# Kernel optimization log

Hardware: AMD Instinct MI355X
Metric: run time of the kernel (lower is better)

Reference implementation:

```python
import jax, jax.numpy as jnp
import numpy as np

T = 300  # windowsize = windowstep(50) * windowmul(6)
D_IN = 39
H1, H2 = 35, 30
FC1, FC2, OUT = 50, 40, 2


def _lstm_layer(x_tbd, W, b, H):
    """TF LSTMCell: gates ordered i, j, f, o; forget_bias=1.0; tanh activation.
    x_tbd: [T, B, D]; W: [D+H, 4H]; b: [4H]. Returns hidden states [T, B, H]."""
    B = x_tbd.shape[1]
    h0 = jnp.zeros((B, H), x_tbd.dtype)
    c0 = jnp.zeros((B, H), x_tbd.dtype)

    def step(carry, xt):
        h, c = carry
        z = jnp.concatenate([xt, h], axis=-1) @ W + b  # [B, 4H]
        i, j, f, o = jnp.split(z, 4, axis=-1)
        c = jax.nn.sigmoid(f + 1.0) * c + jax.nn.sigmoid(i) * jnp.tanh(j)
        h = jax.nn.sigmoid(o) * jnp.tanh(c)
        return (h, c), h

    _, hs = jax.lax.scan(step, (h0, c0), x_tbd)
    return hs


def _stack(x_tbd, W1, b1, W2, b2):
    h1 = _lstm_layer(x_tbd, W1, b1, H1)
    return _lstm_layer(h1, W2, b2, H2)


def setup_inputs() -> dict:
    key = jax.random.key(0)
    ks = jax.random.split(key, 16)
    B = 4096
    s = lambda fan_in: 1.0 / np.sqrt(fan_in)

    def mat(k, shape):
        return jax.random.normal(k, shape, jnp.float32) * s(shape[0])

    return {
        "x": jax.random.normal(ks[0], (B, T, D_IN), jnp.float32),
        "fw_W1": mat(ks[1], (D_IN + H1, 4 * H1)), "fw_b1": jnp.zeros((4 * H1,), jnp.float32),
        "fw_W2": mat(ks[2], (H1 + H2, 4 * H2)), "fw_b2": jnp.zeros((4 * H2,), jnp.float32),
        "bw_W1": mat(ks[3], (D_IN + H1, 4 * H1)), "bw_b1": jnp.zeros((4 * H1,), jnp.float32),
        "bw_W2": mat(ks[4], (H1 + H2, 4 * H2)), "bw_b2": jnp.zeros((4 * H2,), jnp.float32),
        "W_fc1": mat(ks[5], (2 * H2, FC1)), "b_fc1": jnp.zeros((FC1,), jnp.float32),
        "W_fc2": mat(ks[6], (FC1, FC2)), "b_fc2": jnp.zeros((FC2,), jnp.float32),
        "W_out": mat(ks[7], (FC2, OUT)), "b_out": jnp.zeros((OUT,), jnp.float32),
    }


def reference(x, fw_W1, fw_b1, fw_W2, fw_b2, bw_W1, bw_b1, bw_W2, bw_b2,
              W_fc1, b_fc1, W_fc2, b_fc2, W_out, b_out):
    x_tbd = jnp.transpose(x, (1, 0, 2))  # [T, B, D]
    h_fw = _stack(x_tbd, fw_W1, fw_b1, fw_W2, fw_b2)               # [T, B, H2]
    h_bw = _stack(x_tbd[::-1], bw_W1, bw_b1, bw_W2, bw_b2)[::-1]   # [T, B, H2]
    h = jnp.concatenate([h_fw, h_bw], axis=-1)  # [T, B, 2*H2]
    h = jnp.transpose(h, (1, 0, 2))             # [B, T, 60]
    h = jax.nn.relu(h @ W_fc1 + b_fc1)
    h = jax.nn.relu(h @ W_fc2 + b_fc2)
    logits = h @ W_out + b_out                  # [B, T, 2]
    return logits
```

## Files before the change

### kernel.cpp

```cpp
#include <hip/hip_runtime.h>


#define T_STEPS 300
#define DIN 39
#define H1 35
#define H2 30
#define BATCH 4096
#define FC1N 50
#define FC2N 40

#define PAN_STR 136

typedef _Float16 f16;
typedef _Float16 half8 __attribute__((ext_vector_type(8)));
typedef float floatx4 __attribute__((ext_vector_type(4)));

__device__ __forceinline__ float sigf(float x) {
    return __builtin_amdgcn_rcpf(1.0f + __expf(-x));
}
__device__ __forceinline__ float sig_tanh(float a, float b) {
    float bc = fminf(b, 30.0f);
    float ea = __expf(-a);
    float E  = __expf(2.0f * bc);
    return (E - 1.0f) * __builtin_amdgcn_rcpf((1.0f + ea) * (E + 1.0f));
}

__global__ void wprep_kernel(const float* __restrict__ fw1, const float* __restrict__ bw1,
                             const float* __restrict__ fw2, const float* __restrict__ bw2,
                             f16* __restrict__ bp) {
    int frag = blockIdx.x;
    int lane = threadIdx.x;
    int dir = frag / 60;
    int rem = frag % 60;
    int layer = (rem < 36) ? 0 : 1;
    int r2 = (layer == 0) ? rem : rem - 36;
    int ug = r2 / 12, g = (r2 % 12) / 3, c = r2 % 3;
    int u = ug * 16 + (lane & 15);
    const float* W = (layer == 0) ? (dir ? bw1 : fw1) : (dir ? bw2 : fw2);
    for (int j = 0; j < 8; ++j) {
        int k = c * 32 + (lane >> 4) * 8 + j;
        float v = 0.0f;
        if (layer == 0) {
            if (u < H1) {
                int kr = (k < 39) ? k : ((k >= 40 && k < 75) ? k - 1 : -1);
                if (kr >= 0) v = W[kr * (4 * H1) + g * H1 + u];
            }
        } else {
            if (u < H2 && k < 65) v = W[k * (4 * H2) + g * H2 + u];
        }
        bp[(size_t)frag * 512 + lane * 8 + j] = (f16)v;
    }
}

__global__ void fcwprep_kernel(const float* __restrict__ Wf1, const float* __restrict__ Wf2,
                               const float* __restrict__ Wo, f16* __restrict__ fcp) {
    int f = blockIdx.x;
    int lane = threadIdx.x;
    int lm = lane & 15, oct = lane >> 4;
    for (int j = 0; j < 8; ++j) {
        float v = 0.0f;
        if (f < 8) {
            int tile = f >> 1, chunk = f & 1;
            int n = tile * 16 + lm;
            int kl = oct * 8 + j;
            if (n < FC1N && kl < 30) v = Wf1[(chunk * 30 + kl) * FC1N + n];
        } else if (f < 14) {
            int g = f - 8, tile = g >> 1, chunk = g & 1;
            int n = tile * 16 + lm;
            int k = chunk * 32 + oct * 8 + j;
            if (n < FC2N && k < FC1N) v = Wf2[k * FC2N + n];
        } else {
            int chunk = f - 14;
            int k = chunk * 32 + oct * 8 + j;
            if (lm < 2 && k < FC2N) v = Wo[k * 2 + lm];
        }
        fcp[(size_t)f * 512 + lane * 8 + j] = (f16)v;
    }
}

__global__ __launch_bounds__(320, 3) void lstm_fused(
    const float* __restrict__ x, const f16* __restrict__ bp,
    const float* __restrict__ fb1, const float* __restrict__ bb1,
    const float* __restrict__ fb2, const float* __restrict__ bb2,
    f16* __restrict__ h2s)
{
    __shared__ f16 pan[2][16 * PAN_STR];

    const int tid = threadIdx.x;
    const int b0  = blockIdx.x * 16;
    const int dir = blockIdx.y;
    const int wv   = tid >> 6;
    const int lane = tid & 63;
    const int lm = lane & 15, oct = lane >> 4;
    const bool isL2 = (wv >= 3);
    const int ug = isL2 ? (wv - 3) : wv;
    const int u  = ug * 16 + lm;
    const int Hn = isL2 ? H2 : H1;
    const float* bias = isL2 ? (dir ? bb2 : fb2) : (dir ? bb1 : fb1);
    const int fragbase = dir * 60 + (isL2 ? 36 : 0) + ug * 12;

    half8 bf[4][3];
    #pragma unroll
    for (int g = 0; g < 4; ++g)
        #pragma unroll
        for (int c = 0; c < 3; ++c)
            bf[g][c] = *(const half8*)(bp + (size_t)(fragbase + g * 3 + c) * 512 + lane * 8);

    float zb[4];
    #pragma unroll
    for (int g = 0; g < 4; ++g)
        zb[g] = (u < Hn) ? bias[g * Hn + u] : 0.f;
    float cst[4] = {0.f, 0.f, 0.f, 0.f};

    f16* h2p = h2s + ((size_t)(dir * BATCH + b0 + oct * 4) * T_STEPS
                      + (dir ? (T_STEPS - 1) : 0)) * 32 + u;
    const int h2step = dir ? -32 : 32;

    for (int idx = tid; idx < 16 * PAN_STR; idx += 320) {
        pan[0][idx] = (f16)0.f; pan[1][idx] = (f16)0.f;
    }
    __syncthreads();

    const int sr = tid / 10, sq = tid % 10;
    float xv[4] = {0.f, 0.f, 0.f, 0.f};
    if (tid < 160) {
        int t0 = dir ? (T_STEPS - 1) : 0;
        const float* p0 = x + ((size_t)(b0 + sr) * T_STEPS + t0) * DIN;
        union { f16 h[4]; uint2 u; } pk;
        #pragma unroll
        for (int i = 0; i < 4; ++i) { int k = sq * 4 + i; pk.h[i] = (k < DIN) ? (f16)p0[k] : (f16)0.f; }
        *(uint2*)(&pan[0][sr * PAN_STR + sq * 4]) = pk.u;
        int t1 = dir ? (T_STEPS - 2) : 1;
        const float* p1 = x + ((size_t)(b0 + sr) * T_STEPS + t1) * DIN;
        #pragma unroll
        for (int i = 0; i < 4; ++i) { int k = sq * 4 + i; xv[i] = (k < DIN) ? p1[k] : 0.f; }
    }
    __syncthreads();

    const int arow = lm * PAN_STR + oct * 8 + (isL2 ? 40 : 0);

    if (!isL2) {
        floatx4 C[4];
        #pragma unroll
        for (int g = 0; g < 4; ++g) C[g] = (floatx4){zb[g], zb[g], zb[g], zb[g]};
        half8 a0 = *(const half8*)(&pan[0][arow]);
        half8 a1 = *(const half8*)(&pan[0][arow + 32]);
        half8 a2 = *(const half8*)(&pan[0][arow + 64]);
        #pragma unroll
        for (int g = 0; g < 4; ++g) {
            C[g] = __builtin_amdgcn_mfma_f32_16x16x32_f16(a0, bf[g][0], C[g], 0, 0, 0);
            C[g] = __builtin_amdgcn_mfma_f32_16x16x32_f16(a1, bf[g][1], C[g], 0, 0, 0);
            C[g] = __builtin_amdgcn_mfma_f32_16x16x32_f16(a2, bf[g][2], C[g], 0, 0, 0);
        }
        #pragma unroll
        for (int r = 0; r < 4; ++r) {
            float cc = sigf(C[2][r] + 1.0f) * cst[r] + sig_tanh(C[0][r], C[1][r]);
            cst[r] = cc;
            float hh = sig_tanh(C[3][r], cc);
            if (u < H1) {
                int row = oct * 4 + r;
                pan[1][row * PAN_STR + 40 + u] = (f16)hh;
            }
        }
    }
    const float* px = x + ((size_t)(b0 + sr) * T_STEPS
                           + (dir ? (T_STEPS - 4) : 3)) * DIN + sq * 4;
    const int xstep = dir ? -DIN : DIN;
    if (tid < 160) {
        union { f16 h[4]; uint2 u; } pk;
        #pragma unroll
        for (int i = 0; i < 4; ++i) pk.h[i] = (f16)xv[i];
        *(uint2*)(&pan[1][sr * PAN_STR + sq * 4]) = pk.u;
        int t2 = dir ? (T_STEPS - 3) : 2;
        const float* p2 = x + ((size_t)(b0 + sr) * T_STEPS + t2) * DIN;
        #pragma unroll
        for (int i = 0; i < 4; ++i) { int k = sq * 4 + i; xv[i] = (k < DIN) ? p2[k] : 0.f; }
    }
    __syncthreads();

    for (int s = 0; s < T_STEPS; ++s) {
        const int p = 1 - (s & 1);

        float xn[4] = {0.f, 0.f, 0.f, 0.f};
        if (tid < 160) {
            #pragma unroll
            for (int i = 0; i < 4; ++i) { int k = sq * 4 + i; xn[i] = (k < DIN) ? px[i] : 0.f; }
        }
        if (s < T_STEPS - 4) px += xstep;

        const f16* ap = &pan[p][0];
        floatx4 C[4];
        #pragma unroll
        for (int g = 0; g < 4; ++g) C[g] = (floatx4){zb[g], zb[g], zb[g], zb[g]};
        {
            half8 a0 = *(const half8*)(ap + arow);
            half8 a1 = *(const half8*)(ap + arow + 32);
            half8 a2 = *(const half8*)(ap + arow + 64);
            #pragma unroll
            for (int g = 0; g < 4; ++g) {
                C[g] = __builtin_amdgcn_mfma_f32_16x16x32_f16(a0, bf[g][0], C[g], 0, 0, 0);
                C[g] = __builtin_amdgcn_mfma_f32_16x16x32_f16(a1, bf[g][1], C[g], 0, 0, 0);
                C[g] = __builtin_amdgcn_mfma_f32_16x16x32_f16(a2, bf[g][2], C[g], 0, 0, 0);
            }
        }

        f16* w = &pan[1 - p][0];
        if (!isL2) {
            #pragma unroll
            for (int r = 0; r < 4; ++r) {
                float cc = sigf(C[2][r] + 1.0f) * cst[r] + sig_tanh(C[0][r], C[1][r]);
                cst[r] = cc;
                float hh = sig_tanh(C[3][r], cc);
                if (u < H1) {
                    int row = oct * 4 + r;
                    w[row * PAN_STR + 40 + u] = (f16)hh;
                }
            }
        } else {
            #pragma unroll
            for (int r = 0; r < 4; ++r) {
                float dd = sigf(C[2][r] + 1.0f) * cst[r] + sig_tanh(C[0][r], C[1][r]);
                cst[r] = dd;
                float gg = sig_tanh(C[3][r], dd);
                int row = oct * 4 + r;
                f16 gv = (f16)gg;
                w[row * PAN_STR + 75 + u] = gv;
                h2p[(size_t)r * T_STEPS * 32] = gv;
            }
        }
        h2p += h2step;

        if (tid < 160) {
            union { f16 h[4]; uint2 u; } pk;
            #pragma unroll
            for (int i = 0; i < 4; ++i) pk.h[i] = (f16)xv[i];
            *(uint2*)(&pan[1 - p][sr * PAN_STR + sq * 4]) = pk.u;
            #pragma unroll
            for (int i = 0; i < 4; ++i) xv[i] = xn[i];
        }
        __syncthreads();
    }
}

__global__ __launch_bounds__(256) void fc_kernel(
    const f16* __restrict__ h2s, const f16* __restrict__ fcp,
    const float* __restrict__ bf1, const float* __restrict__ bf2,
    const float* __restrict__ bo, float* __restrict__ out)
{
    __shared__ f16 apf[4][2][16 * 72];
    const int tid = threadIdx.x;
    const int wv = tid >> 6, lane = tid & 63;
    const int lm = lane & 15, oct = lane >> 4;
    f16* pa = &apf[wv][0][0];
    f16* pb = &apf[wv][1][0];

    {
        uint* z = (uint*)pa;
        for (int i = lane; i < 1152; i += 64) z[i] = 0u;
    }

    half8 wf[16];
    #pragma unroll
    for (int f = 0; f < 16; ++f)
        wf[f] = *(const half8*)(fcp + (size_t)f * 512 + lane * 8);

    const int ar = lm * 72 + oct * 8;
    const size_t base = (size_t)blockIdx.x * 256 + wv * 64;
    const size_t bwoff = (size_t)BATCH * T_STEPS * 32;

    union U8 { uint4 u; half8 h; };
    const f16* gp = h2s + (base + lm) * 32 + oct * 8;
    U8 va, vb;
    va.u = *(const uint4*)gp;
    vb.u = *(const uint4*)(gp + bwoff);

    for (int it = 0; it < 4; ++it) {
        half8 a0 = va.h, a1 = vb.h;
        if (it < 3) {
            const f16* gn = gp + (size_t)(it + 1) * 16 * 32;
            va.u = *(const uint4*)gn;
            vb.u = *(const uint4*)(gn + bwoff);
        }

        floatx4 C[4];
        #pragma unroll
        for (int t = 0; t < 4; ++t) {
            int col = t * 16 + lm;
            float b = (col < FC1N) ? bf1[col] : 0.f;
            C[t] = (floatx4){b, b, b, b};
            C[t] = __builtin_amdgcn_mfma_f32_16x16x32_f16(a0, wf[t * 2 + 0], C[t], 0, 0, 0);
            C[t] = __builtin_amdgcn_mfma_f32_16x16x32_f16(a1, wf[t * 2 + 1], C[t], 0, 0, 0);
        }
        #pragma unroll
        for (int t = 0; t < 4; ++t) {
            int col = t * 16 + lm;
            #pragma unroll
            for (int r = 0; r < 4; ++r)
                pa[(oct * 4 + r) * 72 + col] = (f16)fmaxf(C[t][r], 0.f);
        }

        half8 b0 = *(const half8*)(pa + ar);
        half8 b1 = *(const half8*)(pa + ar + 32);
        floatx4 D[3];
        #pragma unroll
        for (int t = 0; t < 3; ++t) {
            int col = t * 16 + lm;
            float b = (col < FC2N) ? bf2[col] : 0.f;
            D[t] = (floatx4){b, b, b, b};
            D[t] = __builtin_amdgcn_mfma_f32_16x16x32_f16(b0, wf[8 + t * 2 + 0], D[t], 0, 0, 0);
            D[t] = __builtin_amdgcn_mfma_f32_16x16x32_f16(b1, wf[8 + t * 2 + 1], D[t], 0, 0, 0);
        }
        #pragma unroll
        for (int t = 0; t < 3; ++t) {
            int col = t * 16 + lm;
            #pragma unroll
            for (int r = 0; r < 4; ++r)
                pb[(oct * 4 + r) * 72 + col] = (f16)fmaxf(D[t][r], 0.f);
        }

        half8 c0 = *(const half8*)(pb + ar);
        half8 c1 = *(const half8*)(pb + ar + 32);
        float b = (lm < 2) ? bo[lm] : 0.f;
        floatx4 E = (floatx4){b, b, b, b};
        E = __builtin_amdgcn_mfma_f32_16x16x32_f16(c0, wf[14], E, 0, 0, 0);
        E = __builtin_amdgcn_mfma_f32_16x16x32_f16(c1, wf[15], E, 0, 0, 0);
        if (lm < 2) {
            const size_t rid0 = base + it * 16;
            #pragma unroll
            for (int r = 0; r < 4; ++r)
                out[(rid0 + oct * 4 + r) * 2 + lm] = E[r];
        }
    }
}

extern "C" void kernel_launch(void* const* d_in, const int* in_sizes, int n_in,
                              void* d_out, int out_size, void* d_ws, size_t ws_size,
                              hipStream_t stream) {
    const float* x     = (const float*)d_in[0];
    const float* fw_W1 = (const float*)d_in[1];
    const float* fw_b1 = (const float*)d_in[2];
    const float* fw_W2 = (const float*)d_in[3];
    const float* fw_b2 = (const float*)d_in[4];
    const float* bw_W1 = (const float*)d_in[5];
    const float* bw_b1 = (const float*)d_in[6];
    const float* bw_W2 = (const float*)d_in[7];
    const float* bw_b2 = (const float*)d_in[8];
    const float* Wf1   = (const float*)d_in[9];
    const float* bf1   = (const float*)d_in[10];
    const float* Wf2   = (const float*)d_in[11];
    const float* bf2   = (const float*)d_in[12];
    const float* Wo    = (const float*)d_in[13];
    const float* bo    = (const float*)d_in[14];
    float* outp = (float*)d_out;

    f16* h2s = (f16*)d_ws;
    f16* bp  = h2s + (size_t)2 * BATCH * T_STEPS * 32;
    f16* fcp = bp + (size_t)120 * 512;

    wprep_kernel<<<120, 64, 0, stream>>>(fw_W1, bw_W1, fw_W2, bw_W2, bp);
    fcwprep_kernel<<<16, 64, 0, stream>>>(Wf1, Wf2, Wo, fcp);

    dim3 gl(BATCH / 16, 2);
    lstm_fused<<<gl, 320, 0, stream>>>(x, bp, fw_b1, bw_b1, fw_b2, bw_b2, h2s);

    fc_kernel<<<(BATCH * T_STEPS) / 256, 256, 0, stream>>>(
        h2s, fcp, bf1, bf2, bo, outp);
}
```

Measured before the change: 699.4 us.

## Process 32 batch rows per LSTM block with two interleaved MFMA tiles

Measured after the change: 803.8 us. 14.9% more time.

```diff
diff --git a/kernel.cpp b/kernel.cpp
--- a/kernel.cpp
+++ b/kernel.cpp
@@ -10,6 +10,7 @@
 #define FC2N 40
 
 #define PAN_STR 136
+#define ROWS 32
 
 typedef _Float16 f16;
 typedef _Float16 half8 __attribute__((ext_vector_type(8)));
@@ -78,16 +79,16 @@
     }
 }
 
-__global__ __launch_bounds__(320, 3) void lstm_fused(
+__global__ __launch_bounds__(320, 1) void lstm_fused(
     const float* __restrict__ x, const f16* __restrict__ bp,
     const float* __restrict__ fb1, const float* __restrict__ bb1,
     const float* __restrict__ fb2, const float* __restrict__ bb2,
     f16* __restrict__ h2s)
 {
-    __shared__ f16 pan[2][16 * PAN_STR];
+    __shared__ f16 pan[2][ROWS * PAN_STR];
 
     const int tid = threadIdx.x;
-    const int b0  = blockIdx.x * 16;
+    const int b0  = blockIdx.x * ROWS;
     const int dir = blockIdx.y;
     const int wv   = tid >> 6;
     const int lane = tid & 63;
@@ -110,20 +111,22 @@
     #pragma unroll
     for (int g = 0; g < 4; ++g)
         zb[g] = (u < Hn) ? bias[g * Hn + u] : 0.f;
-    float cst[4] = {0.f, 0.f, 0.f, 0.f};
+    float cs1[4] = {0.f, 0.f, 0.f, 0.f};
+    float cs2[4] = {0.f, 0.f, 0.f, 0.f};
 
     f16* h2p = h2s + ((size_t)(dir * BATCH + b0 + oct * 4) * T_STEPS
                       + (dir ? (T_STEPS - 1) : 0)) * 32 + u;
+    f16* h2q = h2p + (size_t)16 * T_STEPS * 32;
     const int h2step = dir ? -32 : 32;
 
-    for (int idx = tid; idx < 16 * PAN_STR; idx += 320) {
+    for (int idx = tid; idx < ROWS * PAN_STR; idx += 320) {
         pan[0][idx] = (f16)0.f; pan[1][idx] = (f16)0.f;
     }
     __syncthreads();
 
     const int sr = tid / 10, sq = tid % 10;
-    float xv[4] = {0.f, 0.f, 0.f, 0.f};
-    if (tid < 160) {
+    float xv[4];
+    {
         int t0 = dir ? (T_STEPS - 1) : 0;
         const float* p0 = x + ((size_t)(b0 + sr) * T_STEPS + t0) * DIN;
         union { f16 h[4]; uint2 u; } pk;
@@ -137,36 +140,50 @@
     }
     __syncthreads();
 
-    const int arow = lm * PAN_STR + oct * 8 + (isL2 ? 40 : 0);
+    const int arow1 = lm * PAN_STR + oct * 8 + (isL2 ? 40 : 0);
+    const int arow2 = arow1 + 16 * PAN_STR;
 
     if (!isL2) {
-        floatx4 C[4];
-        #pragma unroll
-        for (int g = 0; g < 4; ++g) C[g] = (floatx4){zb[g], zb[g], zb[g], zb[g]};
-        half8 a0 = *(const half8*)(&pan[0][arow]);
-        half8 a1 = *(const half8*)(&pan[0][arow + 32]);
-        half8 a2 = *(const half8*)(&pan[0][arow + 64]);
+        floatx4 C1[4], C2[4];
         #pragma unroll
         for (int g = 0; g < 4; ++g) {
-            C[g] = __builtin_amdgcn_mfma_f32_16x16x32_f16(a0, bf[g][0], C[g], 0, 0, 0);
-            C[g] = __builtin_amdgcn_mfma_f32_16x16x32_f16(a1, bf[g][1], C[g], 0, 0, 0);
-            C[g] = __builtin_amdgcn_mfma_f32_16x16x32_f16(a2, bf[g][2], C[g], 0, 0, 0);
+            C1[g] = (floatx4){zb[g], zb[g], zb[g], zb[g]};
+            C2[g] = C1[g];
+        }
+        half8 a10 = *(const half8*)(&pan[0][arow1]);
+        half8 a11 = *(const half8*)(&pan[0][arow1 + 32]);
+        half8 a12 = *(const half8*)(&pan[0][arow1 + 64]);
+        half8 a20 = *(const half8*)(&pan[0][arow2]);
+        half8 a21 = *(const half8*)(&pan[0][arow2 + 32]);
+        half8 a22 = *(const half8*)(&pan[0][arow2 + 64]);
+        #pragma unroll
+        for (int g = 0; g < 4; ++g) {
+            C1[g] = __builtin_amdgcn_mfma_f32_16x16x32_f16(a10, bf[g][0], C1[g], 0, 0, 0);
+            C1[g] = __builtin_amdgcn_mfma_f32_16x16x32_f16(a11, bf[g][1], C1[g], 0, 0, 0);
+            C1[g] = __builtin_amdgcn_mfma_f32_16x16x32_f16(a12, bf[g][2], C1[g], 0, 0, 0);
+            C2[g] = __builtin_amdgcn_mfma_f32_16x16x32_f16(a20, bf[g][0], C2[g], 0, 0, 0);
+            C2[g] = __builtin_amdgcn_mfma_f32_16x16x32_f16(a21, bf[g][1], C2[g], 0, 0, 0);
+            C2[g] = __builtin_amdgcn_mfma_f32_16x16x32_f16(a22, bf[g][2], C2[g], 0, 0, 0);
         }
         #pragma unroll
         for (int r = 0; r < 4; ++r) {
-            float cc = sigf(C[2][r] + 1.0f) * cst[r] + sig_tanh(C[0][r], C[1][r]);
-            cst[r] = cc;
-            float hh = sig_tanh(C[3][r], cc);
+            float cc = sigf(C1[2][r] + 1.0f) * cs1[r] + sig_tanh(C1[0][r], C1[1][r]);
+            cs1[r] = cc;
+            float hh = sig_tanh(C1[3][r], cc);
+            float cc2 = sigf(C2[2][r] + 1.0f) * cs2[r] + sig_tanh(C2[0][r], C2[1][r]);
+            cs2[r] = cc2;
+            float hh2 = sig_tanh(C2[3][r], cc2);
             if (u < H1) {
                 int row = oct * 4 + r;
                 pan[1][row * PAN_STR + 40 + u] = (f16)hh;
+                pan[1][(16 + row) * PAN_STR + 40 + u] = (f16)hh2;
             }
         }
     }
     const float* px = x + ((size_t)(b0 + sr) * T_STEPS
                            + (dir ? (T_STEPS - 4) : 3)) * DIN + sq * 4;
     const int xstep = dir ? -DIN : DIN;
-    if (tid < 160) {
+    {
         union { f16 h[4]; uint2 u; } pk;
         #pragma unroll
         for (int i = 0; i < 4; ++i) pk.h[i] = (f16)xv[i];
@@ -181,56 +198,71 @@
     for (int s = 0; s < T_STEPS; ++s) {
         const int p = 1 - (s & 1);
 
-        float xn[4] = {0.f, 0.f, 0.f, 0.f};
-        if (tid < 160) {
-            #pragma unroll
-            for (int i = 0; i < 4; ++i) { int k = sq * 4 + i; xn[i] = (k < DIN) ? px[i] : 0.f; }
-        }
+        float xn[4];
+        #pragma unroll
+        for (int i = 0; i < 4; ++i) { int k = sq * 4 + i; xn[i] = (k < DIN) ? px[i] : 0.f; }
         if (s < T_STEPS - 4) px += xstep;
 
         const f16* ap = &pan[p][0];
-        floatx4 C[4];
-        #pragma unroll
-        for (int g = 0; g < 4; ++g) C[g] = (floatx4){zb[g], zb[g], zb[g], zb[g]};
-        {
-            half8 a0 = *(const half8*)(ap + arow);
-            half8 a1 = *(const half8*)(ap + arow + 32);
-            half8 a2 = *(const half8*)(ap + arow + 64);
-            #pragma unroll
-            for (int g = 0; g < 4; ++g) {
-                C[g] = __builtin_amdgcn_mfma_f32_16x16x32_f16(a0, bf[g][0], C[g], 0, 0, 0);
-                C[g] = __builtin_amdgcn_mfma_f32_16x16x32_f16(a1, bf[g][1], C[g], 0, 0, 0);
-                C[g] = __builtin_amdgcn_mfma_f32_16x16x32_f16(a2, bf[g][2], C[g], 0, 0, 0);
-            }
+        half8 a10 = *(const half8*)(ap + arow1);
+        half8 a11 = *(const half8*)(ap + arow1 + 32);
+        half8 a12 = *(const half8*)(ap + arow1 + 64);
+        half8 a20 = *(const half8*)(ap + arow2);
+        half8 a21 = *(const half8*)(ap + arow2 + 32);
+        half8 a22 = *(const half8*)(ap + arow2 + 64);
+        floatx4 C1[4], C2[4];
+        #pragma unroll
+        for (int g = 0; g < 4; ++g) {
+            C1[g] = (floatx4){zb[g], zb[g], zb[g], zb[g]};
+            C2[g] = C1[g];
+        }
+        #pragma unroll
+        for (int g = 0; g < 4; ++g) {
+            C1[g] = __builtin_amdgcn_mfma_f32_16x16x32_f16(a10, bf[g][0], C1[g], 0, 0, 0);
+            C1[g] = __builtin_amdgcn_mfma_f32_16x16x32_f16(a11, bf[g][1], C1[g], 0, 0, 0);
+            C1[g] = __builtin_amdgcn_mfma_f32_16x16x32_f16(a12, bf[g][2], C1[g], 0, 0, 0);
+            C2[g] = __builtin_amdgcn_mfma_f32_16x16x32_f16(a20, bf[g][0], C2[g], 0, 0, 0);
+            C2[g] = __builtin_amdgcn_mfma_f32_16x16x32_f16(a21, bf[g][1], C2[g], 0, 0, 0);
+            C2[g] = __builtin_amdgcn_mfma_f32_16x16x32_f16(a22, bf[g][2], C2[g], 0, 0, 0);
         }
 
         f16* w = &pan[1 - p][0];
         if (!isL2) {
             #pragma unroll
             for (int r = 0; r < 4; ++r) {
-                float cc = sigf(C[2][r] + 1.0f) * cst[r] + sig_tanh(C[0][r], C[1][r]);
-                cst[r] = cc;
-                float hh = sig_tanh(C[3][r], cc);
+                float cc = sigf(C1[2][r] + 1.0f) * cs1[r] + sig_tanh(C1[0][r], C1[1][r]);
+                cs1[r] = cc;
+                float hh = sig_tanh(C1[3][r], cc);
+                float cc2 = sigf(C2[2][r] + 1.0f) * cs2[r] + sig_tanh(C2[0][r], C2[1][r]);
+                cs2[r] = cc2;
+                float hh2 = sig_tanh(C2[3][r], cc2);
                 if (u < H1) {
                     int row = oct * 4 + r;
                     w[row * PAN_STR + 40 + u] = (f16)hh;
+                    w[(16 + row) * PAN_STR + 40 + u] = (f16)hh2;
                 }
             }
         } else {
             #pragma unroll
             for (int r = 0; r < 4; ++r) {
-                float dd = sigf(C[2][r] + 1.0f) * cst[r] + sig_tanh(C[0][r], C[1][r]);
-                cst[r] = dd;
-                float gg = sig_tanh(C[3][r], dd);
+                float dd = sigf(C1[2][r] + 1.0f) * cs1[r] + sig_tanh(C1[0][r], C1[1][r]);
+                cs1[r] = dd;
+                float gg = sig_tanh(C1[3][r], dd);
+                float dd2 = sigf(C2[2][r] + 1.0f) * cs2[r] + sig_tanh(C2[0][r], C2[1][r]);
+                cs2[r] = dd2;
+                float gg2 = sig_tanh(C2[3][r], dd2);
                 int row = oct * 4 + r;
-                f16 gv = (f16)gg;
+                f16 gv = (f16)gg, gv2 = (f16)gg2;
                 w[row * PAN_STR + 75 + u] = gv;
+                w[(16 + row) * PAN_STR + 75 + u] = gv2;
                 h2p[(size_t)r * T_STEPS * 32] = gv;
+                h2q[(size_t)r * T_STEPS * 32] = gv2;
             }
         }
         h2p += h2step;
-
-        if (tid < 160) {
+        h2q += h2step;
+
+        {
             union { f16 h[4]; uint2 u; } pk;
             #pragma unroll
             for (int i = 0; i < 4; ++i) pk.h[i] = (f16)xv[i];
@@ -360,7 +392,7 @@
     wprep_kernel<<<120, 64, 0, stream>>>(fw_W1, bw_W1, fw_W2, bw_W2, bp);
     fcwprep_kernel<<<16, 64, 0, stream>>>(Wf1, Wf2, Wo, fcp);
 
-    dim3 gl(BATCH / 16, 2);
+    dim3 gl(BATCH / ROWS, 2);
     lstm_fused<<<gl, 320, 0, stream>>>(x, bp, fw_b1, bw_b1, fw_b2, bw_b2, h2s);
 
     fc_kernel<<<(BATCH * T_STEPS) / 256, 256, 0, stream>>>(
```

## Fold LSTM bias into GEMM via constant-one column and merge cell gate math

Applied to the files above, without the earlier changes.

Result: slower. 718.1 us (+2.7%).

```diff
diff --git a/kernel.cpp b/kernel.cpp
--- a/kernel.cpp
+++ b/kernel.cpp
@@ -15,18 +15,28 @@
 typedef _Float16 half8 __attribute__((ext_vector_type(8)));
 typedef float floatx4 __attribute__((ext_vector_type(4)));
 
-__device__ __forceinline__ float sigf(float x) {
-    return __builtin_amdgcn_rcpf(1.0f + __expf(-x));
-}
 __device__ __forceinline__ float sig_tanh(float a, float b) {
     float bc = fminf(b, 30.0f);
     float ea = __expf(-a);
     float E  = __expf(2.0f * bc);
     return (E - 1.0f) * __builtin_amdgcn_rcpf((1.0f + ea) * (E + 1.0f));
 }
+__device__ __forceinline__ float cell_update(float i, float j, float f, float cst) {
+    float ef = __expf(-(f + 1.0f));
+    float ei = __expf(-i);
+    float jc = fminf(j, 30.0f);
+    float E  = __expf(2.0f * jc);
+    float Df = 1.0f + ef;
+    float Di = 1.0f + ei;
+    float m  = Di * (E + 1.0f);
+    float num = cst * m + (E - 1.0f) * Df;
+    return num * __builtin_amdgcn_rcpf(Df * m);
+}
 
 __global__ void wprep_kernel(const float* __restrict__ fw1, const float* __restrict__ bw1,
                              const float* __restrict__ fw2, const float* __restrict__ bw2,
+                             const float* __restrict__ fb1, const float* __restrict__ bb1,
+                             const float* __restrict__ fb2, const float* __restrict__ bb2,
                              f16* __restrict__ bp) {
     int frag = blockIdx.x;
     int lane = threadIdx.x;
@@ -37,16 +47,21 @@
     int ug = r2 / 12, g = (r2 % 12) / 3, c = r2 % 3;
     int u = ug * 16 + (lane & 15);
     const float* W = (layer == 0) ? (dir ? bw1 : fw1) : (dir ? bw2 : fw2);
+    const float* B = (layer == 0) ? (dir ? bb1 : fb1) : (dir ? bb2 : fb2);
     for (int j = 0; j < 8; ++j) {
         int k = c * 32 + (lane >> 4) * 8 + j;
         float v = 0.0f;
         if (layer == 0) {
             if (u < H1) {
-                int kr = (k < 39) ? k : ((k >= 40 && k < 75) ? k - 1 : -1);
-                if (kr >= 0) v = W[kr * (4 * H1) + g * H1 + u];
+                if (k < 39)                 v = W[k * (4 * H1) + g * H1 + u];
+                else if (k == 39)           v = B[g * H1 + u];
+                else if (k >= 40 && k < 75) v = W[(k - 1) * (4 * H1) + g * H1 + u];
             }
         } else {
-            if (u < H2 && k < 65) v = W[k * (4 * H2) + g * H2 + u];
+            if (u < H2) {
+                if (k < 65)       v = W[k * (4 * H2) + g * H2 + u];
+                else if (k == 65) v = B[g * H2 + u];
+            }
         }
         bp[(size_t)frag * 512 + lane * 8 + j] = (f16)v;
     }
@@ -80,8 +95,6 @@
 
 __global__ __launch_bounds__(320, 3) void lstm_fused(
     const float* __restrict__ x, const f16* __restrict__ bp,
-    const float* __restrict__ fb1, const float* __restrict__ bb1,
-    const float* __restrict__ fb2, const float* __restrict__ bb2,
     f16* __restrict__ h2s)
 {
     __shared__ f16 pan[2][16 * PAN_STR];
@@ -95,8 +108,6 @@
     const bool isL2 = (wv >= 3);
     const int ug = isL2 ? (wv - 3) : wv;
     const int u  = ug * 16 + lm;
-    const int Hn = isL2 ? H2 : H1;
-    const float* bias = isL2 ? (dir ? bb2 : fb2) : (dir ? bb1 : fb1);
     const int fragbase = dir * 60 + (isL2 ? 36 : 0) + ug * 12;
 
     half8 bf[4][3];
@@ -106,10 +117,6 @@
         for (int c = 0; c < 3; ++c)
             bf[g][c] = *(const half8*)(bp + (size_t)(fragbase + g * 3 + c) * 512 + lane * 8);
 
-    float zb[4];
-    #pragma unroll
-    for (int g = 0; g < 4; ++g)
-        zb[g] = (u < Hn) ? bias[g * Hn + u] : 0.f;
     float cst[4] = {0.f, 0.f, 0.f, 0.f};
 
     f16* h2p = h2s + ((size_t)(dir * BATCH + b0 + oct * 4) * T_STEPS
@@ -120,6 +127,10 @@
         pan[0][idx] = (f16)0.f; pan[1][idx] = (f16)0.f;
     }
     __syncthreads();
+    if (tid < 16) {
+        pan[0][tid * PAN_STR + 105] = (f16)1.f;
+        pan[1][tid * PAN_STR + 105] = (f16)1.f;
+    }
 
     const int sr = tid / 10, sq = tid % 10;
     float xv[4] = {0.f, 0.f, 0.f, 0.f};
@@ -128,33 +139,32 @@
         const float* p0 = x + ((size_t)(b0 + sr) * T_STEPS + t0) * DIN;
         union { f16 h[4]; uint2 u; } pk;
         #pragma unroll
-        for (int i = 0; i < 4; ++i) { int k = sq * 4 + i; pk.h[i] = (k < DIN) ? (f16)p0[k] : (f16)0.f; }
+        for (int i = 0; i < 4; ++i) { int k = sq * 4 + i; pk.h[i] = (k < DIN) ? (f16)p0[k] : (f16)1.f; }
         *(uint2*)(&pan[0][sr * PAN_STR + sq * 4]) = pk.u;
         int t1 = dir ? (T_STEPS - 2) : 1;
         const float* p1 = x + ((size_t)(b0 + sr) * T_STEPS + t1) * DIN;
         #pragma unroll
-        for (int i = 0; i < 4; ++i) { int k = sq * 4 + i; xv[i] = (k < DIN) ? p1[k] : 0.f; }
+        for (int i = 0; i < 4; ++i) { int k = sq * 4 + i; xv[i] = (k < DIN) ? p1[k] : 1.f; }
     }
     __syncthreads();
 
     const int arow = lm * PAN_STR + oct * 8 + (isL2 ? 40 : 0);
+    const floatx4 Z0 = (floatx4){0.f, 0.f, 0.f, 0.f};
 
     if (!isL2) {
         floatx4 C[4];
-        #pragma unroll
-        for (int g = 0; g < 4; ++g) C[g] = (floatx4){zb[g], zb[g], zb[g], zb[g]};
         half8 a0 = *(const half8*)(&pan[0][arow]);
         half8 a1 = *(const half8*)(&pan[0][arow + 32]);
         half8 a2 = *(const half8*)(&pan[0][arow + 64]);
         #pragma unroll
         for (int g = 0; g < 4; ++g) {
-            C[g] = __builtin_amdgcn_mfma_f32_16x16x32_f16(a0, bf[g][0], C[g], 0, 0, 0);
+            C[g] = __builtin_amdgcn_mfma_f32_16x16x32_f16(a0, bf[g][0], Z0, 0, 0, 0);
             C[g] = __builtin_amdgcn_mfma_f32_16x16x32_f16(a1, bf[g][1], C[g], 0, 0, 0);
             C[g] = __builtin_amdgcn_mfma_f32_16x16x32_f16(a2, bf[g][2], C[g], 0, 0, 0);
         }
         #pragma unroll
         for (int r = 0; r < 4; ++r) {
-            float cc = sigf(C[2][r] + 1.0f) * cst[r] + sig_tanh(C[0][r], C[1][r]);
+            float cc = cell_update(C[0][r], C[1][r], C[2][r], cst[r]);
             cst[r] = cc;
             float hh = sig_tanh(C[3][r], cc);
             if (u < H1) {
@@ -174,41 +184,40 @@
         int t2 = dir ? (T_STEPS - 3) : 2;
         const float* p2 = x + ((size_t)(b0 + sr) * T_STEPS + t2) * DIN;
         #pragma unroll
-        for (int i = 0; i < 4; ++i) { int k = sq * 4 + i; xv[i] = (k < DIN) ? p2[k] : 0.f; }
+        for (int i = 0; i < 4; ++i) { int k = sq * 4 + i; xv[i] = (k < DIN) ? p2[k] : 1.f; }
     }
     __syncthreads();
 
     for (int s = 0; s < T_STEPS; ++s) {
         const int p = 1 - (s & 1);
 
-        float xn[4] = {0.f, 0.f, 0.f, 0.f};
+        float xn[4] = {1.f, 1.f, 1.f, 1.f};
         if (tid < 160) {
             #pragma unroll
-            for (int i = 0; i < 4; ++i) { int k = sq * 4 + i; xn[i] = (k < DIN) ? px[i] : 0.f; }
+            for (int i = 0; i < 4; ++i) { int k = sq * 4 + i; xn[i] = (k < DIN) ? px[i] : 1.f; }
         }
         if (s < T_STEPS - 4) px += xstep;
 
         const f16* ap = &pan[p][0];
         floatx4 C[4];
-        #pragma unroll
-        for (int g = 0; g < 4; ++g) C[g] = (floatx4){zb[g], zb[g], zb[g], zb[g]};
         {
             half8 a0 = *(const half8*)(ap + arow);
             half8 a1 = *(const half8*)(ap + arow + 32);
             half8 a2 = *(const half8*)(ap + arow + 64);
             #pragma unroll
             for (int g = 0; g < 4; ++g) {
-                C[g] = __builtin_amdgcn_mfma_f32_16x16x32_f16(a0, bf[g][0], C[g], 0, 0, 0);
+                C[g] = __builtin_amdgcn_mfma_f32_16x16x32_f16(a0, bf[g][0], Z0, 0, 0, 0);
                 C[g] = __builtin_amdgcn_mfma_f32_16x16x32_f16(a1, bf[g][1], C[g], 0, 0, 0);
                 C[g] = __builtin_amdgcn_mfma_f32_16x16x32_f16(a2, bf[g][2], C[g], 0, 0, 0);
             }
         }
 
         f16* w = &pan[1 - p][0];
+        __builtin_amdgcn_s_setprio(1);
         if (!isL2) {
             #pragma unroll
             for (int r = 0; r < 4; ++r) {
-                float cc = sigf(C[2][r] + 1.0f) * cst[r] + sig_tanh(C[0][r], C[1][r]);
+                float cc = cell_update(C[0][r], C[1][r], C[2][r], cst[r]);
                 cst[r] = cc;
                 float hh = sig_tanh(C[3][r], cc);
                 if (u < H1) {
@@ -219,15 +228,16 @@
         } else {
             #pragma unroll
             for (int r = 0; r < 4; ++r) {
-                float dd = sigf(C[2][r] + 1.0f) * cst[r] + sig_tanh(C[0][r], C[1][r]);
+                float dd = cell_update(C[0][r], C[1][r], C[2][r], cst[r]);
                 cst[r] = dd;
                 float gg = sig_tanh(C[3][r], dd);
                 int row = oct * 4 + r;
                 f16 gv = (f16)gg;
-                w[row * PAN_STR + 75 + u] = gv;
+                if (u < H2) w[row * PAN_STR + 75 + u] = gv;
                 h2p[(size_t)r * T_STEPS * 32] = gv;
             }
         }
+        __builtin_amdgcn_s_setprio(0);
         h2p += h2step;
 
         if (tid < 160) {
@@ -357,11 +367,12 @@
     f16* bp  = h2s + (size_t)2 * BATCH * T_STEPS * 32;
     f16* fcp = bp + (size_t)120 * 512;
 
-    wprep_kernel<<<120, 64, 0, stream>>>(fw_W1, bw_W1, fw_W2, bw_W2, bp);
+    wprep_kernel<<<120, 64, 0, stream>>>(fw_W1, bw_W1, fw_W2, bw_W2,
+                                         fw_b1, bw_b1, fw_b2, bw_b2, bp);
     fcwprep_kernel<<<16, 64, 0, stream>>>(Wf1, Wf2, Wo, fcp);
 
     dim3 gl(BATCH / 16, 2);
-    lstm_fused<<<gl, 320, 0, stream>>>(x, bp, fw_b1, bw_b1, fw_b2, bw_b2, h2s);
+    lstm_fused<<<gl, 320, 0, stream>>>(x, bp, h2s);
 
     fc_kernel<<<(BATCH * T_STEPS) / 256, 256, 0, stream>>>(
         h2s, fcp, bf1, bf2, bo, outp);
```
